# Kernel tuning notes

Measured on AMD Instinct MI355X. Metric: run time of the kernel, lower is better.

Reference implementation:

```python
import jax, jax.numpy as jnp
import numpy as np

# Problem dimensions (see shape_source)
N_TOTAL = 2048   # canonical nodes in batch
M = 8            # subgraphs per canonical node
K = 16           # sampled nodes per subgraph
S = N_TOTAL * M  # 16384 subgraphs
F = S * K        # 262144 flat nodes
E = 1048576      # intra-subgraph edges (64 per subgraph)
G = 128          # graphs in batch
D = 64           # hidden_dim
H = 4            # num_heads
DH = D // H
MAX_DIST = 32
NUM_LAYERS = 4
IN_CH = 119
EDGE_DIM = 5


def setup_inputs() -> dict:
    key = jax.random.key(0)
    ks = jax.random.split(key, 24)
    x_idx = jax.random.randint(ks[0], (F,), 0, IN_CH)
    edge_attr_idx = jax.random.randint(ks[1], (E,), 1, EDGE_DIM + 1)  # bond labels 1..5 (code does -1)
    # edges stay inside their subgraph: 64 edges per subgraph
    eps = E // S
    sub_of_edge = jnp.arange(E) // eps
    src = sub_of_edge * K + jax.random.randint(ks[2], (E,), 0, K)
    dst = sub_of_edge * K + jax.random.randint(ks[3], (E,), 0, K)
    node_ids = jax.random.randint(ks[4], (F,), 0, N_TOTAL)
    drop = jax.random.uniform(ks[5], (F,)) < 0.1
    is_root = (jnp.arange(F) % K) == 0
    node_ids = jnp.where(drop & (~is_root), -1, node_ids)
    node_ids = jnp.where(is_root, jnp.arange(F) // (K * M), node_ids)
    lp = -3.0 * jax.random.uniform(ks[6], (S,))  # log sampling probs (finite, negative)
    batch = jnp.sort(jax.random.randint(ks[7], (N_TOTAL,), 0, G))
    s = 0.02
    atom_emb = s * jax.random.normal(ks[8], (IN_CH, D))
    bond_emb = s * jax.random.normal(ks[9], (EDGE_DIM, D))
    dist_emb = s * jax.random.normal(ks[10], (MAX_DIST + 1, D))
    logp_w = s * jax.random.normal(ks[11], (1, D))
    logp_b = jnp.zeros((D,))
    mlp_w1 = s * jax.random.normal(ks[12], (NUM_LAYERS, D, D))
    mlp_b1 = jnp.zeros((NUM_LAYERS, D))
    mlp_w2 = s * jax.random.normal(ks[13], (NUM_LAYERS, D, D))
    mlp_b2 = jnp.zeros((NUM_LAYERS, D))
    ht_alpha = jnp.ones((1,))
    in_proj_w = s * jax.random.normal(ks[14], (3 * D, D))
    in_proj_b = jnp.zeros((3 * D,))
    out_proj_w = s * jax.random.normal(ks[15], (D, D))
    out_proj_b = jnp.zeros((D,))
    bn_gamma = jnp.ones((D,))
    bn_beta = jnp.zeros((D,))
    return {
        'x_idx': x_idx, 'edge_attr_idx': edge_attr_idx, 'src': src, 'dst': dst,
        'node_ids': node_ids, 'lp': lp, 'batch': batch,
        'atom_emb': atom_emb, 'bond_emb': bond_emb, 'dist_emb': dist_emb,
        'logp_w': logp_w, 'logp_b': logp_b,
        'mlp_w1': mlp_w1, 'mlp_b1': mlp_b1, 'mlp_w2': mlp_w2, 'mlp_b2': mlp_b2,
        'ht_alpha': ht_alpha, 'in_proj_w': in_proj_w, 'in_proj_b': in_proj_b,
        'out_proj_w': out_proj_w, 'out_proj_b': out_proj_b,
        'bn_gamma': bn_gamma, 'bn_beta': bn_beta,
    }


def reference(x_idx, edge_attr_idx, src, dst, node_ids, lp, batch,
              atom_emb, bond_emb, dist_emb, logp_w, logp_b,
              mlp_w1, mlp_b1, mlp_w2, mlp_b2, ht_alpha,
              in_proj_w, in_proj_b, out_proj_w, out_proj_b,
              bn_gamma, bn_beta):
    # --- embed nodes / bonds ---
    x_flat = atom_emb[x_idx]                       # [F, D]
    ea = bond_emb[edge_attr_idx - 1]               # [E, D]
    sub_batch = jnp.arange(F) // K                 # flat node -> subgraph id
    root = jnp.arange(S) * K
    # --- BFS distances from each subgraph root (edge relaxation, MAX_DIST iters) ---
    big = jnp.int32(MAX_DIST + K)
    d0 = jnp.full((F,), big, dtype=jnp.int32).at[root].set(0)
    def bfs_step(d, _):
        return d.at[dst].min(d[src] + 1), None
    dist, _ = jax.lax.scan(bfs_step, d0, None, length=MAX_DIST)
    dist = jnp.minimum(dist, MAX_DIST)
    dist_pe = dist_emb[dist]                       # [F, D]
    # --- log-prob positional encoding ---
    lp_s = jnp.where(jnp.isfinite(lp), lp, 0.0)    # [S]
    logp_pe = jax.nn.relu(lp_s[sub_batch][:, None] * logp_w[0][None, :] + logp_b)
    valid = node_ids >= 0
    vf = valid[:, None].astype(x_flat.dtype)
    h = (x_flat + dist_pe + logp_pe) * vf          # [F, D]
    # --- GINE-style message passing layers (Arch9Layer assumed: sum-aggregate ReLU(h_src+e) -> 2-layer MLP, residual, validity mask) ---
    for l in range(NUM_LAYERS):
        msg = jax.nn.relu(h[src] + ea)             # [E, D]
        agg = jax.ops.segment_sum(msg, dst, num_segments=F)
        z = jax.nn.relu(agg @ mlp_w1[l] + mlp_b1[l]) @ mlp_w2[l] + mlp_b2[l]
        h = (h + z) * vf
    # --- per-subgraph sum readout ---
    h_sub = jax.ops.segment_sum(h * vf, sub_batch, num_segments=S)  # [S, D]
    h3 = h_sub.reshape(N_TOTAL, M, D)
    # --- HT-biased multihead attention over the m subgraphs of each node ---
    bias = (-ht_alpha[0] * lp_s.reshape(N_TOTAL, M))[:, None, None, :]  # key-only bias [N,1,1,m]
    qkv = h3 @ in_proj_w.T + in_proj_b
    q, k_, v = jnp.split(qkv, 3, axis=-1)
    q = q.reshape(N_TOTAL, M, H, DH)
    k_ = k_.reshape(N_TOTAL, M, H, DH)
    v = v.reshape(N_TOTAL, M, H, DH)
    scores = jnp.einsum('nqhd,nkhd->nhqk', q, k_) / np.sqrt(DH).astype(np.float32) + bias
    attn = jax.nn.softmax(scores, axis=-1)
    o = jnp.einsum('nhqk,nkhd->nqhd', attn, v).reshape(N_TOTAL, M, D)
    o = o @ out_proj_w.T + out_proj_b
    h_attn = o + h3
    # --- mean over subgraphs, batchnorm (training-mode batch stats), graph pooling ---
    pooled = h_attn.mean(axis=1)                   # [N_TOTAL, D]
    mu = pooled.mean(axis=0)
    var = pooled.var(axis=0)
    node_emb = (pooled - mu) / jnp.sqrt(var + 1e-5) * bn_gamma + bn_beta
    return jax.ops.segment_sum(node_emb, batch, num_segments=G)   # [G, D]
```

## Files before the change

### kernel.cpp

```cpp
#include <hip/hip_runtime.h>
#include <hip/hip_bf16.h>

typedef __hip_bfloat16 bf16;
typedef __attribute__((ext_vector_type(8))) _Float16 f16x8;
typedef __attribute__((ext_vector_type(4))) float f32x4;
typedef __attribute__((ext_vector_type(4))) unsigned u32x4;

#define N_TOTAL 2048
#define M_SUB   8
#define KN      16
#define S_SUB   16384
#define F_NODES 262144
#define E_EDGES 1048576
#define G_GRAPHS 128
#define D_DIM   64
#define EPS_SUB 64

#define H_ROWB  144
#define B_ROWB  272

__device__ __forceinline__ float b2f(bf16 x) { return __bfloat162float(x); }
__device__ __forceinline__ float bfu2f(unsigned short u) {
    return __uint_as_float(((unsigned)u) << 16);
}

__device__ __forceinline__ bool get_isbf(const void* alpha) {
    return ((const unsigned short*)alpha)[0] == 0x3F80;
}
__device__ __forceinline__ float ldf(const void* p, int i, bool isbf) {
    if (isbf) return __bfloat162float(((const bf16*)p)[i]);
    return ((const float*)p)[i];
}
__device__ __forceinline__ unsigned f2bf(float x) {
    return (unsigned)__builtin_bit_cast(unsigned short, __float2bfloat16(x));
}
__device__ __forceinline__ unsigned pkrtz(float a, float b) {
    unsigned r;
    asm("v_cvt_pkrtz_f16_f32 %0, %1, %2" : "=v"(r) : "v"(a), "v"(b));
    return r;
}
__device__ __forceinline__ unsigned pk_add_f16(unsigned a, unsigned b) {
    unsigned r;
    asm("v_pk_add_f16 %0, %1, %2" : "=v"(r) : "v"(a), "v"(b));
    return r;
}
__device__ __forceinline__ unsigned pk_max0_f16(unsigned a, unsigned z) {
    unsigned r;
    asm("v_pk_max_f16 %0, %1, %2" : "=v"(r) : "v"(a), "v"(z));
    return r;
}
__device__ __forceinline__ unsigned f2h(float x) {
    unsigned r;
    asm("v_cvt_f16_f32 %0, %1" : "=v"(r) : "v"(x));
    return r;
}
__device__ __forceinline__ unsigned pack_lo(unsigned a, unsigned b) {
    return (a & 0xFFFFu) | (b << 16);
}
__device__ __forceinline__ unsigned pack_hi(unsigned a, unsigned b) {
    return (a >> 16) | (b & 0xFFFF0000u);
}

__global__ __launch_bounds__(256) void k_prew(
    const void* __restrict__ mlp_w1, const void* __restrict__ mlp_w2,
    const void* __restrict__ alpha_p, unsigned short* __restrict__ wb)
{
    const bool isbf = get_isbf(alpha_p);
    int t = blockIdx.x * 256 + threadIdx.x;
    int L   = t >> 13;
    int rem = t & 8191;
    int mi  = rem >> 12;
    int wdx = rem & 4095;
    int row = wdx >> 6, col = wdx & 63;
    int kb = row >> 5, c = col >> 4;
    int f  = kb * 4 + c;
    int lane_ = (((row >> 3) & 3) << 4) | (col & 15);
    int u  = row & 7;
    float val = ldf(mi ? mlp_w2 : mlp_w1, L * 4096 + wdx, isbf);
    _Float16 hv = (_Float16)val;
    wb[((((L * 2 + mi) * 8 + f) * 64 + lane_) << 3) + u] = __builtin_bit_cast(unsigned short, hv);
}

__global__ __launch_bounds__(256) void k_subgraph(
    const int* __restrict__ x_idx, const int* __restrict__ eattr,
    const int* __restrict__ src, const int* __restrict__ dst,
    const int* __restrict__ node_ids, const void* __restrict__ lp,
    const void* __restrict__ atom_emb, const void* __restrict__ bond_emb,
    const void* __restrict__ dist_emb, const void* __restrict__ logp_w,
    const void* __restrict__ logp_b,
    const void* __restrict__ mlp_b1, const void* __restrict__ mlp_b2,
    const void* __restrict__ alpha_p,
    const unsigned short* __restrict__ wbg,
    float* __restrict__ hsub)
{
    __shared__ __align__(16) unsigned short sh_h[4][KN][72];
    __shared__ __align__(16) unsigned short ab_f16[4][KN*72];
    __shared__ __align__(16) float sh_bond[5 * 68];
    __shared__ int   sh_im[4][16];
    __shared__ int   sh_dist[4][16];
    __shared__ float sh_vf[4][16];
    __shared__ int   sh_xi[4][16];

    const int tid = threadIdx.x;
    const int w   = tid >> 6;
    const int j   = tid & 63;
    const int s   = blockIdx.x * 4 + w;
    const int q   = j & 15, g = j >> 4;
    const bool isbf = get_isbf(alpha_p);

    if (isbf) {
        const bf16* bp = (const bf16*)bond_emb;
        for (int t = tid; t < 5 * 64; t += 256) {
            int a = t >> 6, ch = t & 63;
            sh_bond[a * 68 + (ch & 15) * 4 + (ch >> 4)] = b2f(bp[t]);
        }
    } else {
        const float* bp = (const float*)bond_emb;
        for (int t = tid; t < 5 * 64; t += 256) {
            int a = t >> 6, ch = t & 63;
            sh_bond[a * 68 + (ch & 15) * 4 + (ch >> 4)] = bp[t];
        }
    }

    int eidx = s * EPS_SUB + j;
    int esrc = src[eidx]  - s * KN;
    int edst = dst[eidx]  - s * KN;
    int ea   = eattr[eidx] - 1;

    if (j < KN) {
        int f = s * KN + j;
        sh_xi[w][j]  = x_idx[f];
        sh_vf[w][j]  = (node_ids[f] >= 0) ? 1.0f : 0.0f;
        sh_im[w][j]  = 0;
    }
    __syncthreads();

    atomicOr(&sh_im[w][edst], 1 << esrc);

    unsigned pk = (unsigned)(esrc * H_ROWB) | ((unsigned)edst << 12)
                | ((unsigned)(ea * B_ROWB) << 16);
    const unsigned qq16 = (unsigned)(q * 8) | (((unsigned)(q * 16)) << 16);
    unsigned d0[8], d1[8];
    u32x4 ic0, ic1;
    #pragma unroll
    for (int up = 0; up < 4; ++up) {
        unsigned pa = (unsigned)__shfl((int)pk, 8 * g + 2 * up);
        unsigned pb = (unsigned)__shfl((int)pk, 8 * g + 2 * up + 1);
        unsigned pc = (unsigned)__shfl((int)pk, 32 + 8 * g + 2 * up);
        unsigned pd = (unsigned)__shfl((int)pk, 32 + 8 * g + 2 * up + 1);
        d0[2*up]   = (pa & 0xFFFF0FFFu) + qq16;
        d0[2*up+1] = (pb & 0xFFFF0FFFu) + qq16;
        d1[2*up]   = (pc & 0xFFFF0FFFu) + qq16;
        d1[2*up+1] = (pd & 0xFFFF0FFFu) + qq16;
        ic0[up] = ((((pa >> 12) & 15u) == (unsigned)q) ? 0x3C00u : 0u)
                | ((((pb >> 12) & 15u) == (unsigned)q) ? 0x3C000000u : 0u);
        ic1[up] = ((((pc >> 12) & 15u) == (unsigned)q) ? 0x3C00u : 0u)
                | ((((pd >> 12) & 15u) == (unsigned)q) ? 0x3C000000u : 0u);
    }
    const f16x8 incf0 = __builtin_bit_cast(f16x8, ic0);
    const f16x8 incf1 = __builtin_bit_cast(f16x8, ic1);

    {
        int inm  = (j < 16) ? sh_im[w][j] : 0;
        int dist = (j == 0) ? 0 : 48;
        unsigned reached = 1u;
        #pragma unroll
        for (int t = 1; t < 16; ++t) {
            bool r = (inm & (int)reached) != 0;
            unsigned long long b = __ballot(r);
            if (r && dist == 48) dist = t;
            reached |= (unsigned)(b & 0xFFFFu);
        }
        if (j < 16) sh_dist[w][j] = dist;
    }

    float vfr[4]; int xi4[4], di4[4];
    #pragma unroll
    for (int r = 0; r < 4; ++r) {
        int n = 4 * g + r;
        vfr[r] = sh_vf[w][n];
        xi4[r] = sh_xi[w][n];
        int d  = sh_dist[w][n];
        di4[r] = d > 32 ? 32 : d;
    }

    char* const hbase = (char*)&sh_h[w][0][0];
    const char* const bondb = (const char*)sh_bond;

    unsigned bpk0[4][4], bpk1[4][4];
    #pragma unroll
    for (int up = 0; up < 4; ++up) {
        {
            float4 ba = *(const float4*)(bondb + (d0[2*up] >> 16));
            float4 bb = *(const float4*)(bondb + (d0[2*up+1] >> 16));
            bpk0[0][up] = pkrtz(ba.x, bb.x);
            bpk0[1][up] = pkrtz(ba.y, bb.y);
            bpk0[2][up] = pkrtz(ba.z, bb.z);
            bpk0[3][up] = pkrtz(ba.w, bb.w);
        }
        {
            float4 ba = *(const float4*)(bondb + (d1[2*up] >> 16));
            float4 bb = *(const float4*)(bondb + (d1[2*up+1] >> 16));
            bpk1[0][up] = pkrtz(ba.x, bb.x);
            bpk1[1][up] = pkrtz(ba.y, bb.y);
            bpk1[2][up] = pkrtz(ba.z, bb.z);
            bpk1[3][up] = pkrtz(ba.w, bb.w);
        }
    }

    float hreg[4][4];
    {
        const float lp_s = ldf(lp, s, isbf);
        if (isbf) {
            const bf16* ap = (const bf16*)atom_emb;
            const bf16* dp = (const bf16*)dist_emb;
            const bf16* wp = (const bf16*)logp_w;
            const bf16* bp = (const bf16*)logp_b;
            #pragma unroll
            for (int c = 0; c < 4; ++c) {
                int ch = c * 16 + q;
                float lpe = fmaxf(lp_s * b2f(wp[ch]) + b2f(bp[ch]), 0.0f);
                #pragma unroll
                for (int r = 0; r < 4; ++r)
                    hreg[c][r] = (b2f(ap[xi4[r] * 64 + ch]) + b2f(dp[di4[r] * 64 + ch]) + lpe) * vfr[r];
            }
        } else {
            const float* ap = (const float*)atom_emb;
            const float* dp = (const float*)dist_emb;
            const float* wp = (const float*)logp_w;
            const float* bp = (const float*)logp_b;
            #pragma unroll
            for (int c = 0; c < 4; ++c) {
                int ch = c * 16 + q;
                float lpe = fmaxf(lp_s * wp[ch] + bp[ch], 0.0f);
                #pragma unroll
                for (int r = 0; r < 4; ++r)
                    hreg[c][r] = (ap[xi4[r] * 64 + ch] + dp[di4[r] * 64 + ch] + lpe) * vfr[r];
            }
        }
        #pragma unroll
        for (int r = 0; r < 4; ++r) {
            uint2 v;
            v.x = pkrtz(hreg[0][r], hreg[1][r]);
            v.y = pkrtz(hreg[2][r], hreg[3][r]);
            *(uint2*)(hbase + (4 * g + r) * H_ROWB + q * 8) = v;
        }
    }

    const f16x8* wbv = (const f16x8*)wbg;
    const unsigned zz = 0u;

    for (int L = 0; L < 4; ++L) {
        float b1c[4], b2c[4];
        if (isbf) {
            const bf16* p1 = (const bf16*)mlp_b1 + L * 64 + q;
            const bf16* p2 = (const bf16*)mlp_b2 + L * 64 + q;
            #pragma unroll
            for (int c = 0; c < 4; ++c) { b1c[c] = b2f(p1[c * 16]); b2c[c] = b2f(p2[c * 16]); }
        } else {
            const float* p1 = (const float*)mlp_b1 + L * 64 + q;
            const float* p2 = (const float*)mlp_b2 + L * 64 + q;
            #pragma unroll
            for (int c = 0; c < 4; ++c) { b1c[c] = p1[c * 16]; b2c[c] = p2[c * 16]; }
        }

        u32x4 mb0[4], mb1[4];
        #pragma unroll
        for (int up = 0; up < 4; ++up) {
            uint2 ha = *(const uint2*)(hbase + (d0[2*up] & 0xFFFFu));
            uint2 hb = *(const uint2*)(hbase + (d0[2*up+1] & 0xFFFFu));
            mb0[0][up] = pk_max0_f16(pk_add_f16(pack_lo(ha.x, hb.x), bpk0[0][up]), zz);
            mb0[1][up] = pk_max0_f16(pk_add_f16(pack_hi(ha.x, hb.x), bpk0[1][up]), zz);
            mb0[2][up] = pk_max0_f16(pk_add_f16(pack_lo(ha.y, hb.y), bpk0[2][up]), zz);
            mb0[3][up] = pk_max0_f16(pk_add_f16(pack_hi(ha.y, hb.y), bpk0[3][up]), zz);
        }
        #pragma unroll
        for (int up = 0; up < 4; ++up) {
            uint2 ha = *(const uint2*)(hbase + (d1[2*up] & 0xFFFFu));
            uint2 hb = *(const uint2*)(hbase + (d1[2*up+1] & 0xFFFFu));
            mb1[0][up] = pk_max0_f16(pk_add_f16(pack_lo(ha.x, hb.x), bpk1[0][up]), zz);
            mb1[1][up] = pk_max0_f16(pk_add_f16(pack_hi(ha.x, hb.x), bpk1[1][up]), zz);
            mb1[2][up] = pk_max0_f16(pk_add_f16(pack_lo(ha.y, hb.y), bpk1[2][up]), zz);
            mb1[3][up] = pk_max0_f16(pk_add_f16(pack_hi(ha.y, hb.y), bpk1[3][up]), zz);
        }

        #pragma unroll
        for (int c = 0; c < 4; ++c) {
            f32x4 acc = {0.f, 0.f, 0.f, 0.f};
            acc = __builtin_amdgcn_mfma_f32_16x16x32_f16(incf0, __builtin_bit_cast(f16x8, mb0[c]), acc, 0, 0, 0);
            acc = __builtin_amdgcn_mfma_f32_16x16x32_f16(incf1, __builtin_bit_cast(f16x8, mb1[c]), acc, 0, 0, 0);
            #pragma unroll
            for (int r = 0; r < 4; ++r)
                ab_f16[w][(4 * g + r) * 72 + c * 16 + q] = (unsigned short)f2h(acc[r]);
        }

        f16x8 a0 = *(const f16x8*)&ab_f16[w][q * 72 + g * 8];
        f16x8 a1 = *(const f16x8*)&ab_f16[w][q * 72 + 32 + g * 8];
        int base1 = ((L * 2 + 0) * 8) * 64 + j;
        int base2 = ((L * 2 + 1) * 8) * 64 + j;
        #pragma unroll
        for (int c = 0; c < 4; ++c) {
            f32x4 acc = {b1c[c], b1c[c], b1c[c], b1c[c]};
            acc = __builtin_amdgcn_mfma_f32_16x16x32_f16(a0, wbv[base1 + c * 64], acc, 0, 0, 0);
            acc = __builtin_amdgcn_mfma_f32_16x16x32_f16(a1, wbv[base1 + (4 + c) * 64], acc, 0, 0, 0);
            #pragma unroll
            for (int r = 0; r < 4; ++r)
                ab_f16[w][(g * 4 + r) * 72 + c * 16 + q] =
                    (unsigned short)f2h(fmaxf(acc[r], 0.0f));
        }

        f16x8 u0 = *(const f16x8*)&ab_f16[w][q * 72 + g * 8];
        f16x8 u1 = *(const f16x8*)&ab_f16[w][q * 72 + 32 + g * 8];
        #pragma unroll
        for (int c = 0; c < 4; ++c) {
            f32x4 acc = {b2c[c], b2c[c], b2c[c], b2c[c]};
            acc = __builtin_amdgcn_mfma_f32_16x16x32_f16(u0, wbv[base2 + c * 64], acc, 0, 0, 0);
            acc = __builtin_amdgcn_mfma_f32_16x16x32_f16(u1, wbv[base2 + (4 + c) * 64], acc, 0, 0, 0);
            #pragma unroll
            for (int r = 0; r < 4; ++r)
                hreg[c][r] = (hreg[c][r] + acc[r]) * vfr[r];
        }
        if (L < 3) {
            #pragma unroll
            for (int r = 0; r < 4; ++r) {
                uint2 v;
                v.x = pkrtz(hreg[0][r], hreg[1][r]);
                v.y = pkrtz(hreg[2][r], hreg[3][r]);
                *(uint2*)(hbase + (4 * g + r) * H_ROWB + q * 8) = v;
            }
        }
    }

    float tot[4];
    #pragma unroll
    for (int c = 0; c < 4; ++c) {
        tot[c] = (hreg[c][0] + hreg[c][1]) + (hreg[c][2] + hreg[c][3]);
        tot[c] += __shfl_xor(tot[c], 16, 64);
        tot[c] += __shfl_xor(tot[c], 32, 64);
    }
    float t01 = (g & 1) ? tot[1] : tot[0];
    float t23 = (g & 1) ? tot[3] : tot[2];
    hsub[s * 64 + j] = (g & 2) ? t23 : t01;
}

__global__ __launch_bounds__(256) void k_attn(
    const float* __restrict__ hsub, const void* __restrict__ lp,
    const void* __restrict__ alpha_p,
    const void* __restrict__ Win, const void* __restrict__ bin,
    const void* __restrict__ Wout, const void* __restrict__ bout,
    float* __restrict__ pooled)
{
    __shared__ unsigned short shWinT[64 * 193];
    __shared__ __align__(16) float sh_h3[4][8][64];
    __shared__ __align__(16) float sh_qkv[4][8][192];
    __shared__ __align__(16) float sh_o[4][8][64];
    __shared__ __align__(16) float sh_ob[4][64];

    const int tid = threadIdx.x;
    const int w   = tid >> 6;
    const int j   = tid & 63;
    const int n   = blockIdx.x * 4 + w;
    const bool isbf = get_isbf(alpha_p);

    if (isbf) {
        const unsigned short* Wp = (const unsigned short*)Win;
        for (int t = tid; t < 192 * 64; t += 256)
            shWinT[(t & 63) * 193 + (t >> 6)] = Wp[t];
    } else {
        const float* Wp = (const float*)Win;
        for (int t = tid; t < 192 * 64; t += 256)
            shWinT[(t & 63) * 193 + (t >> 6)] = (unsigned short)f2bf(Wp[t]);
    }

    for (int m = 0; m < 8; ++m)
        sh_h3[w][m][j] = hsub[(n * 8 + m) * 64 + j];
    __syncthreads();

    float accq[8], acck[8], accv[8];
    {
        const float bq = ldf(bin, j, isbf), bk = ldf(bin, 64 + j, isbf), bv = ldf(bin, 128 + j, isbf);
        #pragma unroll
        for (int m = 0; m < 8; ++m) { accq[m] = bq; acck[m] = bk; accv[m] = bv; }
    }
    #pragma unroll 2
    for (int i4 = 0; i4 < 16; ++i4) {
        float wq[4], wk[4], wv[4];
        #pragma unroll
        for (int u = 0; u < 4; ++u) {
            int i = i4 * 4 + u;
            wq[u] = bfu2f(shWinT[i * 193 + j]);
            wk[u] = bfu2f(shWinT[i * 193 + 64 + j]);
            wv[u] = bfu2f(shWinT[i * 193 + 128 + j]);
        }
        #pragma unroll
        for (int m = 0; m < 8; ++m) {
            const float4 a4 = *reinterpret_cast<const float4*>(&sh_h3[w][m][i4 * 4]);
            accq[m] = fmaf(a4.x, wq[0], accq[m]); accq[m] = fmaf(a4.y, wq[1], accq[m]);
            accq[m] = fmaf(a4.z, wq[2], accq[m]); accq[m] = fmaf(a4.w, wq[3], accq[m]);
            acck[m] = fmaf(a4.x, wk[0], acck[m]); acck[m] = fmaf(a4.y, wk[1], acck[m]);
            acck[m] = fmaf(a4.z, wk[2], acck[m]); acck[m] = fmaf(a4.w, wk[3], acck[m]);
            accv[m] = fmaf(a4.x, wv[0], accv[m]); accv[m] = fmaf(a4.y, wv[1], accv[m]);
            accv[m] = fmaf(a4.z, wv[2], accv[m]); accv[m] = fmaf(a4.w, wv[3], accv[m]);
        }
    }
    #pragma unroll
    for (int m = 0; m < 8; ++m) {
        sh_qkv[w][m][j]       = accq[m];
        sh_qkv[w][m][64 + j]  = acck[m];
        sh_qkv[w][m][128 + j] = accv[m];
    }
    __syncthreads();

    if (j < 32) {
        const int hh = j >> 3, m1 = j & 7;
        const float alpha = ldf(alpha_p, 0, isbf);
        float qv[16];
        #pragma unroll
        for (int d = 0; d < 16; ++d) qv[d] = sh_qkv[w][m1][hh * 16 + d];
        float sc[8];
        #pragma unroll
        for (int m2 = 0; m2 < 8; ++m2) {
            float sacc = 0.0f;
            #pragma unroll
            for (int d = 0; d < 16; ++d)
                sacc += qv[d] * sh_qkv[w][m2][64 + hh * 16 + d];
            sc[m2] = sacc * 0.25f - alpha * ldf(lp, n * 8 + m2, isbf);
        }
        float mx = sc[0];
        #pragma unroll
        for (int m2 = 1; m2 < 8; ++m2) mx = fmaxf(mx, sc[m2]);
        float ssum = 0.0f;
        #pragma unroll
        for (int m2 = 0; m2 < 8; ++m2) { sc[m2] = expf(sc[m2] - mx); ssum += sc[m2]; }
        const float inv = 1.0f / ssum;
        #pragma unroll
        for (int m2 = 0; m2 < 8; ++m2) sc[m2] *= inv;
        #pragma unroll
        for (int d = 0; d < 16; ++d) {
            float ov = 0.0f;
            #pragma unroll
            for (int m2 = 0; m2 < 8; ++m2)
                ov += sc[m2] * sh_qkv[w][m2][128 + hh * 16 + d];
            sh_o[w][m1][hh * 16 + d] = ov;
        }
    }
    __syncthreads();

    float obar = 0.0f, h3bar = 0.0f;
    #pragma unroll
    for (int m = 0; m < 8; ++m) { obar += sh_o[w][m][j]; h3bar += sh_h3[w][m][j]; }
    obar *= 0.125f; h3bar *= 0.125f;
    sh_ob[w][j] = obar;

    float acc = ldf(bout, j, isbf) + h3bar;
    if (isbf) {
        const unsigned short* Wrow = (const unsigned short*)Wout + j * 64;
        #pragma unroll 4
        for (int i4 = 0; i4 < 16; ++i4) {
            const float4 o4 = *reinterpret_cast<const float4*>(&sh_ob[w][i4 * 4]);
            const ushort4 wv = *reinterpret_cast<const ushort4*>(&Wrow[i4 * 4]);
            acc = fmaf(o4.x, bfu2f(wv.x), acc);
            acc = fmaf(o4.y, bfu2f(wv.y), acc);
            acc = fmaf(o4.z, bfu2f(wv.z), acc);
            acc = fmaf(o4.w, bfu2f(wv.w), acc);
        }
    } else {
        const float* Wrow = (const float*)Wout + j * 64;
        #pragma unroll 4
        for (int i4 = 0; i4 < 16; ++i4) {
            const float4 o4 = *reinterpret_cast<const float4*>(&sh_ob[w][i4 * 4]);
            const float4 wv = *reinterpret_cast<const float4*>(&Wrow[i4 * 4]);
            acc = fmaf(o4.x, wv.x, acc); acc = fmaf(o4.y, wv.y, acc);
            acc = fmaf(o4.z, wv.z, acc); acc = fmaf(o4.w, wv.w, acc);
        }
    }
    pooled[n * 64 + j] = acc;
}

__global__ __launch_bounds__(256) void k_stats(
    const float* __restrict__ pooled, float* __restrict__ mu, float* __restrict__ rstd)
{
    const int d = blockIdx.x;
    const int t = threadIdx.x;
    float s1 = 0.0f, s2 = 0.0f;
    for (int nn = t; nn < N_TOTAL; nn += 256) {
        float v = pooled[nn * 64 + d];
        s1 += v; s2 += v * v;
    }
    __shared__ float r1[256], r2[256];
    r1[t] = s1; r2[t] = s2;
    __syncthreads();
    for (int o = 128; o > 0; o >>= 1) {
        if (t < o) { r1[t] += r1[t + o]; r2[t] += r2[t + o]; }
        __syncthreads();
    }
    if (t == 0) {
        float m   = r1[0] * (1.0f / N_TOTAL);
        float var = r2[0] * (1.0f / N_TOTAL) - m * m;
        mu[d]   = m;
        rstd[d] = rsqrtf(var + 1e-5f);
    }
}

__global__ __launch_bounds__(64) void k_final(
    const float* __restrict__ pooled, const float* __restrict__ mu,
    const float* __restrict__ rstd, const void* __restrict__ gamma,
    const void* __restrict__ beta, const int* __restrict__ batch,
    const void* __restrict__ alpha_p, void* __restrict__ out)
{
    const int gph = blockIdx.x;
    const int j   = threadIdx.x;
    const bool isbf = get_isbf(alpha_p);

    int a = 0, b = N_TOTAL;
    while (a < b) { int m = (a + b) >> 1; if (batch[m] < gph) a = m + 1; else b = m; }
    const int lo = a;
    b = N_TOTAL;
    while (a < b) { int m = (a + b) >> 1; if (batch[m] < gph + 1) a = m + 1; else b = m; }
    const int hi = a;

    const float mj = mu[j], rj = rstd[j];
    const float gj = ldf(gamma, j, isbf), bj = ldf(beta, j, isbf);
    const float scale = rj * gj;

    float sum = 0.0f;
    for (int nn = lo; nn < hi; ++nn)
        sum += (pooled[nn * 64 + j] - mj) * scale + bj;

    if (isbf) ((bf16*)out)[gph * 64 + j]  = __float2bfloat16(sum);
    else      ((float*)out)[gph * 64 + j] = sum;
}

extern "C" void kernel_launch(void* const* d_in, const int* in_sizes, int n_in,
                              void* d_out, int out_size, void* d_ws, size_t ws_size,
                              hipStream_t stream)
{
    const int*  x_idx    = (const int*) d_in[0];
    const int*  eattr    = (const int*) d_in[1];
    const int*  srcv     = (const int*) d_in[2];
    const int*  dstv     = (const int*) d_in[3];
    const int*  node_ids = (const int*) d_in[4];
    const void* lp       = d_in[5];
    const int*  batch    = (const int*) d_in[6];
    const void* atom_emb = d_in[7];
    const void* bond_emb = d_in[8];
    const void* dist_emb = d_in[9];
    const void* logp_w   = d_in[10];
    const void* logp_b   = d_in[11];
    const void* mlp_w1   = d_in[12];
    const void* mlp_b1   = d_in[13];
    const void* mlp_w2   = d_in[14];
    const void* mlp_b2   = d_in[15];
    const void* ht_alpha = d_in[16];
    const void* Win      = d_in[17];
    const void* bin      = d_in[18];
    const void* Wout     = d_in[19];
    const void* bout     = d_in[20];
    const void* gamma    = d_in[21];
    const void* beta     = d_in[22];

    char* ws = (char*)d_ws;
    float* hsub   = (float*)(ws);
    float* pooled = (float*)(ws + 4194304);
    float* mu     = (float*)(ws + 4718592);
    float* rstd   = (float*)(ws + 4718848);
    unsigned short* wbg = (unsigned short*)(ws + 4751872);

    k_prew<<<128, 256, 0, stream>>>(mlp_w1, mlp_w2, ht_alpha, wbg);

    k_subgraph<<<S_SUB / 4, 256, 0, stream>>>(
        x_idx, eattr, srcv, dstv, node_ids, lp,
        atom_emb, bond_emb, dist_emb, logp_w, logp_b,
        mlp_b1, mlp_b2, ht_alpha, wbg, hsub);

    k_attn<<<N_TOTAL / 4, 256, 0, stream>>>(
        hsub, lp, ht_alpha, Win, bin, Wout, bout, pooled);

    k_stats<<<64, 256, 0, stream>>>(pooled, mu, rstd);

    k_final<<<G_GRAPHS, 64, 0, stream>>>(
        pooled, mu, rstd, gamma, beta, batch, ht_alpha, d_out);
}
```

Measured before the change: 99.36 us.

## Precompute paired bond embeddings in LDS to cut register pressure

Replaces the per-thread register cache of packed bond embeddings (32 registers) with a shared-memory table of all 25 bond-type pairs, pre-packed as f16x2 and loaded once per layer with a single 16-byte LDS read. Edge src/dst offsets are packed two per register, which also shrinks the live register set, and launch bounds now request 4 blocks per SIMD to raise occupancy. In exchange, each layer does extra LDS reads for the bond terms and the block prologue builds a larger table, but far fewer registers stay live across the layer loop.

Result: faster. 96.03 us (median of 3 runs) (-3.3%).

```diff
diff --git a/kernel.cpp b/kernel.cpp
--- a/kernel.cpp
+++ b/kernel.cpp
@@ -17,7 +17,7 @@
 #define EPS_SUB 64
 
 #define H_ROWB  144
-#define B_ROWB  272
+#define BP_ROWB 272
 
 __device__ __forceinline__ float b2f(bf16 x) { return __bfloat162float(x); }
 __device__ __forceinline__ float bfu2f(unsigned short u) {
@@ -81,7 +81,7 @@
     wb[((((L * 2 + mi) * 8 + f) * 64 + lane_) << 3) + u] = __builtin_bit_cast(unsigned short, hv);
 }
 
-__global__ __launch_bounds__(256) void k_subgraph(
+__global__ __launch_bounds__(256, 4) void k_subgraph(
     const int* __restrict__ x_idx, const int* __restrict__ eattr,
     const int* __restrict__ src, const int* __restrict__ dst,
     const int* __restrict__ node_ids, const void* __restrict__ lp,
@@ -95,7 +95,7 @@
 {
     __shared__ __align__(16) unsigned short sh_h[4][KN][72];
     __shared__ __align__(16) unsigned short ab_f16[4][KN*72];
-    __shared__ __align__(16) float sh_bond[5 * 68];
+    __shared__ __align__(16) unsigned sh_bp[25 * 68];
     __shared__ int   sh_im[4][16];
     __shared__ int   sh_dist[4][16];
     __shared__ float sh_vf[4][16];
@@ -109,16 +109,20 @@
     const bool isbf = get_isbf(alpha_p);
 
     if (isbf) {
-        const bf16* bp = (const bf16*)bond_emb;
-        for (int t = tid; t < 5 * 64; t += 256) {
-            int a = t >> 6, ch = t & 63;
-            sh_bond[a * 68 + (ch & 15) * 4 + (ch >> 4)] = b2f(bp[t]);
+        const bf16* bpg = (const bf16*)bond_emb;
+        for (int t = tid; t < 25 * 64; t += 256) {
+            int row = t >> 6, ch = t & 63;
+            int aa = row / 5, ab = row - aa * 5;
+            sh_bp[row * 68 + (ch & 15) * 4 + (ch >> 4)] =
+                pkrtz(b2f(bpg[aa * 64 + ch]), b2f(bpg[ab * 64 + ch]));
         }
     } else {
-        const float* bp = (const float*)bond_emb;
-        for (int t = tid; t < 5 * 64; t += 256) {
-            int a = t >> 6, ch = t & 63;
-            sh_bond[a * 68 + (ch & 15) * 4 + (ch >> 4)] = bp[t];
+        const float* bpg = (const float*)bond_emb;
+        for (int t = tid; t < 25 * 64; t += 256) {
+            int row = t >> 6, ch = t & 63;
+            int aa = row / 5, ab = row - aa * 5;
+            sh_bp[row * 68 + (ch & 15) * 4 + (ch >> 4)] =
+                pkrtz(bpg[aa * 64 + ch], bpg[ab * 64 + ch]);
         }
     }
 
@@ -138,9 +142,9 @@
     atomicOr(&sh_im[w][edst], 1 << esrc);
 
     unsigned pk = (unsigned)(esrc * H_ROWB) | ((unsigned)edst << 12)
-                | ((unsigned)(ea * B_ROWB) << 16);
-    const unsigned qq16 = (unsigned)(q * 8) | (((unsigned)(q * 16)) << 16);
-    unsigned d0[8], d1[8];
+                | ((unsigned)ea << 16);
+    unsigned dpk0[4], dpk1[4];
+    unsigned p0[4], p1[4];
     u32x4 ic0, ic1;
     #pragma unroll
     for (int up = 0; up < 4; ++up) {
@@ -148,10 +152,10 @@
         unsigned pb = (unsigned)__shfl((int)pk, 8 * g + 2 * up + 1);
         unsigned pc = (unsigned)__shfl((int)pk, 32 + 8 * g + 2 * up);
         unsigned pd = (unsigned)__shfl((int)pk, 32 + 8 * g + 2 * up + 1);
-        d0[2*up]   = (pa & 0xFFFF0FFFu) + qq16;
-        d0[2*up+1] = (pb & 0xFFFF0FFFu) + qq16;
-        d1[2*up]   = (pc & 0xFFFF0FFFu) + qq16;
-        d1[2*up+1] = (pd & 0xFFFF0FFFu) + qq16;
+        dpk0[up] = ((pa & 0xFFFu) + q * 8) | (((pb & 0xFFFu) + q * 8) << 16);
+        dpk1[up] = ((pc & 0xFFFu) + q * 8) | (((pd & 0xFFFu) + q * 8) << 16);
+        p0[up] = ((pa >> 16) * 5 + (pb >> 16)) * BP_ROWB + q * 16;
+        p1[up] = ((pc >> 16) * 5 + (pd >> 16)) * BP_ROWB + q * 16;
         ic0[up] = ((((pa >> 12) & 15u) == (unsigned)q) ? 0x3C00u : 0u)
                 | ((((pb >> 12) & 15u) == (unsigned)q) ? 0x3C000000u : 0u);
         ic1[up] = ((((pc >> 12) & 15u) == (unsigned)q) ? 0x3C00u : 0u)
@@ -185,28 +189,7 @@
     }
 
     char* const hbase = (char*)&sh_h[w][0][0];
-    const char* const bondb = (const char*)sh_bond;
-
-    unsigned bpk0[4][4], bpk1[4][4];
-    #pragma unroll
-    for (int up = 0; up < 4; ++up) {
-        {
-            float4 ba = *(const float4*)(bondb + (d0[2*up] >> 16));
-            float4 bb = *(const float4*)(bondb + (d0[2*up+1] >> 16));
-            bpk0[0][up] = pkrtz(ba.x, bb.x);
-            bpk0[1][up] = pkrtz(ba.y, bb.y);
-            bpk0[2][up] = pkrtz(ba.z, bb.z);
-            bpk0[3][up] = pkrtz(ba.w, bb.w);
-        }
-        {
-            float4 ba = *(const float4*)(bondb + (d1[2*up] >> 16));
-            float4 bb = *(const float4*)(bondb + (d1[2*up+1] >> 16));
-            bpk1[0][up] = pkrtz(ba.x, bb.x);
-            bpk1[1][up] = pkrtz(ba.y, bb.y);
-            bpk1[2][up] = pkrtz(ba.z, bb.z);
-            bpk1[3][up] = pkrtz(ba.w, bb.w);
-        }
-    }
+    const char* const bpbase = (const char*)sh_bp;
 
     float hreg[4][4];
     {
@@ -253,35 +236,37 @@
     for (int L = 0; L < 4; ++L) {
         float b1c[4], b2c[4];
         if (isbf) {
-            const bf16* p1 = (const bf16*)mlp_b1 + L * 64 + q;
-            const bf16* p2 = (const bf16*)mlp_b2 + L * 64 + q;
-            #pragma unroll
-            for (int c = 0; c < 4; ++c) { b1c[c] = b2f(p1[c * 16]); b2c[c] = b2f(p2[c * 16]); }
+            const bf16* p1b = (const bf16*)mlp_b1 + L * 64 + q;
+            const bf16* p2b = (const bf16*)mlp_b2 + L * 64 + q;
+            #pragma unroll
+            for (int c = 0; c < 4; ++c) { b1c[c] = b2f(p1b[c * 16]); b2c[c] = b2f(p2b[c * 16]); }
         } else {
-            const float* p1 = (const float*)mlp_b1 + L * 64 + q;
-            const float* p2 = (const float*)mlp_b2 + L * 64 + q;
-            #pragma unroll
-            for (int c = 0; c < 4; ++c) { b1c[c] = p1[c * 16]; b2c[c] = p2[c * 16]; }
+            const float* p1b = (const float*)mlp_b1 + L * 64 + q;
+            const float* p2b = (const float*)mlp_b2 + L * 64 + q;
+            #pragma unroll
+            for (int c = 0; c < 4; ++c) { b1c[c] = p1b[c * 16]; b2c[c] = p2b[c * 16]; }
         }
 
         u32x4 mb0[4], mb1[4];
         #pragma unroll
         for (int up = 0; up < 4; ++up) {
-            uint2 ha = *(const uint2*)(hbase + (d0[2*up] & 0xFFFFu));
-            uint2 hb = *(const uint2*)(hbase + (d0[2*up+1] & 0xFFFFu));
-            mb0[0][up] = pk_max0_f16(pk_add_f16(pack_lo(ha.x, hb.x), bpk0[0][up]), zz);
-            mb0[1][up] = pk_max0_f16(pk_add_f16(pack_hi(ha.x, hb.x), bpk0[1][up]), zz);
-            mb0[2][up] = pk_max0_f16(pk_add_f16(pack_lo(ha.y, hb.y), bpk0[2][up]), zz);
-            mb0[3][up] = pk_max0_f16(pk_add_f16(pack_hi(ha.y, hb.y), bpk0[3][up]), zz);
+            uint2 ha = *(const uint2*)(hbase + (dpk0[up] & 0xFFFFu));
+            uint2 hb = *(const uint2*)(hbase + (dpk0[up] >> 16));
+            u32x4 bp = *(const u32x4*)(bpbase + p0[up]);
+            mb0[0][up] = pk_max0_f16(pk_add_f16(pack_lo(ha.x, hb.x), bp[0]), zz);
+            mb0[1][up] = pk_max0_f16(pk_add_f16(pack_hi(ha.x, hb.x), bp[1]), zz);
+            mb0[2][up] = pk_max0_f16(pk_add_f16(pack_lo(ha.y, hb.y), bp[2]), zz);
+            mb0[3][up] = pk_max0_f16(pk_add_f16(pack_hi(ha.y, hb.y), bp[3]), zz);
         }
         #pragma unroll
         for (int up = 0; up < 4; ++up) {
-            uint2 ha = *(const uint2*)(hbase + (d1[2*up] & 0xFFFFu));
-            uint2 hb = *(const uint2*)(hbase + (d1[2*up+1] & 0xFFFFu));
-            mb1[0][up] = pk_max0_f16(pk_add_f16(pack_lo(ha.x, hb.x), bpk1[0][up]), zz);
-            mb1[1][up] = pk_max0_f16(pk_add_f16(pack_hi(ha.x, hb.x), bpk1[1][up]), zz);
-            mb1[2][up] = pk_max0_f16(pk_add_f16(pack_lo(ha.y, hb.y), bpk1[2][up]), zz);
-            mb1[3][up] = pk_max0_f16(pk_add_f16(pack_hi(ha.y, hb.y), bpk1[3][up]), zz);
+            uint2 ha = *(const uint2*)(hbase + (dpk1[up] & 0xFFFFu));
+            uint2 hb = *(const uint2*)(hbase + (dpk1[up] >> 16));
+            u32x4 bp = *(const u32x4*)(bpbase + p1[up]);
+            mb1[0][up] = pk_max0_f16(pk_add_f16(pack_lo(ha.x, hb.x), bp[0]), zz);
+            mb1[1][up] = pk_max0_f16(pk_add_f16(pack_hi(ha.x, hb.x), bp[1]), zz);
+            mb1[2][up] = pk_max0_f16(pk_add_f16(pack_lo(ha.y, hb.y), bp[2]), zz);
+            mb1[3][up] = pk_max0_f16(pk_add_f16(pack_hi(ha.y, hb.y), bp[3]), zz);
         }
 
         #pragma unroll
```
